# Kernel tuning notes

Hardware: AMD Instinct MI355X
Metric: run time of the kernel (lower is better)

The kernel has to match this reference:

```python
import jax, jax.numpy as jnp
import numpy as np

H = 128   # hidden_dim
M = 8     # mix_dim
N = 20000 # num_nodes
E = 320000

def gelu(x):
    return jax.nn.gelu(x, approximate=False)  # torch F.gelu default is exact erf

def setup_inputs() -> dict:
    key = jax.random.key(0)
    k1, k2, k3, k4 = jax.random.split(key, 4)
    X = jax.random.normal(k1, (N, H), dtype=jnp.float32)
    edge_index = jax.random.randint(k2, (2, E), 0, N, dtype=jnp.int64)
    # Linear weights, torch layout: y = x @ W.T
    W_A = jax.random.normal(k3, (H, H), dtype=jnp.float32) / np.sqrt(H)
    W_B = jax.random.normal(k4, (M, H), dtype=jnp.float32) / np.sqrt(H)
    return {"X": X, "edge_index": edge_index, "W_A": W_A, "W_B": W_B, "num_nodes": N}

def reference(X, edge_index, W_A, W_B, num_nodes):
    src, dst = edge_index[0], edge_index[1]
    X_src = X[src]                                   # (E, h) gather
    # compute_W_tar: W_B(gelu(W_A(X_src))), input_activation=False
    W_tar_edge = gelu(X_src @ W_A.T) @ W_B.T         # (E, m)
    # per-edge outer product, scatter_add over dst
    cross = jnp.einsum('eh,em->ehm', X_src, W_tar_edge)          # (E, h, m)
    agg = jax.ops.segment_sum(cross, dst, num_segments=num_nodes) # (N, h, m)
    agg = gelu(agg)
    # gather agg back to edges, contract over mix dim
    out_edge = jnp.einsum('ehm,em->eh', agg[dst], W_tar_edge)     # (E, h)
    # scatter_mean over dst
    ones = jnp.ones((dst.shape[0],), dtype=X.dtype)
    count = jax.ops.segment_sum(ones, dst, num_segments=num_nodes)
    out_sum = jax.ops.segment_sum(out_edge, dst, num_segments=num_nodes)
    out = out_sum / jnp.maximum(count, 1.0)[:, None]
    return out
```

## Files before the change

kernel.cpp:

```cpp
#include <hip/hip_runtime.h>
#include <hip/hip_bf16.h>


#define H 128
#define MDIM 8
#define CAP 64

typedef float v2f __attribute__((ext_vector_type(2)));

__device__ __forceinline__ float gelu_f(float x) {
    float x2 = x * x;
    float u  = x * (0.7978845608f + 0.0356774081f * x2);
    float u2 = u * u;
    float num = u * (945.0f + u2 * (105.0f + u2));
    float den = 945.0f + u2 * (420.0f + 15.0f * u2);
    float t = num * __builtin_amdgcn_rcpf(den);
    t = fminf(fmaxf(t, -1.0f), 1.0f);
    return 0.5f * (x + x * t);
}

__device__ __forceinline__ v2f gelu2(v2f x) {
    v2f x2 = x * x;
    v2f u  = x * (0.7978845608f + 0.0356774081f * x2);
    v2f u2 = u * u;
    v2f num = u * (945.0f + u2 * (105.0f + u2));
    v2f den = 945.0f + u2 * (420.0f + 15.0f * u2);
    v2f t;
    t.x = num.x * __builtin_amdgcn_rcpf(den.x);
    t.y = num.y * __builtin_amdgcn_rcpf(den.y);
    t.x = fminf(fmaxf(t.x, -1.0f), 1.0f);
    t.y = fminf(fmaxf(t.y, -1.0f), 1.0f);
    return 0.5f * (x + x * t);
}

__global__ __launch_bounds__(128) void k_prep_fill(const float* __restrict__ X,
                                                   const float* __restrict__ WA,
                                                   const float* __restrict__ WB,
                                                   const int* __restrict__ ei,
                                                   float* __restrict__ T,
                                                   int* __restrict__ cnt,
                                                   int* __restrict__ bucket,
                                                   int N, int E) {
    __shared__ float Xs[32][68];
    __shared__ float Ws[128][68];
    __shared__ float WBs[8][132];
    const int t  = threadIdx.x;
    const int n0 = blockIdx.x * 32;
    const int tn = t >> 4;
    const int tj = t & 15;

    #pragma unroll
    for (int i = 0; i < 2; ++i) {
        int idx = t + 128 * i;
        int r = idx >> 5, c4 = idx & 31;
        *(float4*)&WBs[r][c4 * 4] = *(const float4*)(WB + (size_t)r * H + c4 * 4);
    }

    float acc[4][8] = {};

    for (int kh = 0; kh < 2; ++kh) {
        __syncthreads();
        const int kb = kh * 64;
        #pragma unroll
        for (int i = 0; i < 4; ++i) {
            int idx = t + 128 * i;
            int r = idx >> 4, c4 = idx & 15;
            *(float4*)&Xs[r][c4 * 4] =
                *(const float4*)(X + (size_t)(n0 + r) * H + kb + c4 * 4);
        }
        #pragma unroll
        for (int i = 0; i < 16; ++i) {
            int idx = t + 128 * i;
            int r = idx >> 4, c4 = idx & 15;
            *(float4*)&Ws[r][c4 * 4] =
                *(const float4*)(WA + (size_t)r * H + kb + c4 * 4);
        }
        __syncthreads();

        #pragma unroll 1
        for (int k = 0; k < 64; k += 4) {
            float4 xv[4], bv[8];
            #pragma unroll
            for (int nn = 0; nn < 4; ++nn)
                xv[nn] = *(const float4*)&Xs[4 * tn + nn][k];
            #pragma unroll
            for (int jj = 0; jj < 8; ++jj)
                bv[jj] = *(const float4*)&Ws[tj + 16 * jj][k];
            #pragma unroll
            for (int nn = 0; nn < 4; ++nn)
                #pragma unroll
                for (int jj = 0; jj < 8; ++jj)
                    acc[nn][jj] += xv[nn].x * bv[jj].x + xv[nn].y * bv[jj].y +
                                   xv[nn].z * bv[jj].z + xv[nn].w * bv[jj].w;
        }
    }

    __syncthreads();
    float (*Hs)[132] = (float(*)[132])Ws;
    #pragma unroll
    for (int nn = 0; nn < 4; ++nn)
        #pragma unroll
        for (int jj = 0; jj < 8; ++jj)
            Hs[4 * tn + nn][tj + 16 * jj] = gelu_f(acc[nn][jj]);
    __syncthreads();

    #pragma unroll
    for (int i = 0; i < 2; ++i) {
        int q = t + 128 * i;
        int n = q >> 3, m = q & 7;
        float s = 0.f;
        #pragma unroll 4
        for (int kk = 0; kk < 32; ++kk) {
            float4 h = *(const float4*)&Hs[n][kk * 4];
            float4 w = *(const float4*)&WBs[m][kk * 4];
            s += h.x * w.x + h.y * w.y + h.z * w.z + h.w * w.w;
        }
        T[(size_t)(n0 + n) * MDIM + m] = s;
    }

    {
        const int stride = gridDim.x * 128;
        for (int e = blockIdx.x * 128 + t; e < E; e += stride) {
            int s  = ei[e];
            int dd = ei[E + e];
            int p  = atomicAdd(&cnt[dd], 1);
            if (p < CAP) bucket[dd * CAP + p] = s;
        }
    }
}

__device__ __forceinline__ void fma8v(v2f* acc, v2f xv, float4 ta, float4 tb) {
    acc[0] += xv * ta.x;
    acc[1] += xv * ta.y;
    acc[2] += xv * ta.z;
    acc[3] += xv * ta.w;
    acc[4] += xv * tb.x;
    acc[5] += xv * tb.y;
    acc[6] += xv * tb.z;
    acc[7] += xv * tb.w;
}

__global__ __launch_bounds__(256) void k_main(const float* __restrict__ X,
                                              const float* __restrict__ T,
                                              const int* __restrict__ cnt,
                                              const int* __restrict__ bucket,
                                              float* __restrict__ out, int N) {
    __shared__ __attribute__((aligned(16))) int srcs[4][CAP];
    __shared__ float Tl[4][CAP][MDIM];
    const int w    = threadIdx.x >> 6;
    const int lane = threadIdx.x & 63;
    const int d    = blockIdx.x * 4 + w;
    if (d >= N) return;

    const int c  = cnt[d];
    const int cc = (c < CAP) ? c : CAP;

    if (lane < cc) {
        int s = bucket[d * CAP + lane];
        srcs[w][lane] = s;
        const float4* t4 = (const float4*)(T + (size_t)s * MDIM);
        *(float4*)&Tl[w][lane][0] = t4[0];
        *(float4*)&Tl[w][lane][4] = t4[1];
    }

    float sp = 0.f;
    {
        const int m = lane & 7, g = lane >> 3;
        for (int j = g; j < cc; j += 8) sp += Tl[w][j][m];
        sp += __shfl_xor(sp, 8);
        sp += __shfl_xor(sp, 16);
        sp += __shfl_xor(sp, 32);
    }
    float S[MDIM];
    #pragma unroll
    for (int m = 0; m < MDIM; ++m) S[m] = __shfl(sp, m);

    v2f acc[MDIM] = {};
    const float* Xl = X + 2 * lane;

    int j = 0;
    for (; j + 8 <= cc; j += 8) {
        int4 sa = *(const int4*)&srcs[w][j];
        int4 sb = *(const int4*)&srcs[w][j + 4];
        v2f x0 = *(const v2f*)(Xl + (size_t)sa.x * H);
        v2f x1 = *(const v2f*)(Xl + (size_t)sa.y * H);
        v2f x2 = *(const v2f*)(Xl + (size_t)sa.z * H);
        v2f x3 = *(const v2f*)(Xl + (size_t)sa.w * H);
        v2f x4 = *(const v2f*)(Xl + (size_t)sb.x * H);
        v2f x5 = *(const v2f*)(Xl + (size_t)sb.y * H);
        v2f x6 = *(const v2f*)(Xl + (size_t)sb.z * H);
        v2f x7 = *(const v2f*)(Xl + (size_t)sb.w * H);
        #pragma unroll
        for (int q = 0; q < 8; ++q) {
            float4 ta = *(const float4*)&Tl[w][j + q][0];
            float4 tb = *(const float4*)&Tl[w][j + q][4];
            v2f xv = (q == 0) ? x0 : (q == 1) ? x1 : (q == 2) ? x2 : (q == 3) ? x3
                   : (q == 4) ? x4 : (q == 5) ? x5 : (q == 6) ? x6 : x7;
            fma8v(acc, xv, ta, tb);
        }
    }
    for (; j + 4 <= cc; j += 4) {
        int4 s4 = *(const int4*)&srcs[w][j];
        v2f x0 = *(const v2f*)(Xl + (size_t)s4.x * H);
        v2f x1 = *(const v2f*)(Xl + (size_t)s4.y * H);
        v2f x2 = *(const v2f*)(Xl + (size_t)s4.z * H);
        v2f x3 = *(const v2f*)(Xl + (size_t)s4.w * H);
        fma8v(acc, x0, *(const float4*)&Tl[w][j + 0][0], *(const float4*)&Tl[w][j + 0][4]);
        fma8v(acc, x1, *(const float4*)&Tl[w][j + 1][0], *(const float4*)&Tl[w][j + 1][4]);
        fma8v(acc, x2, *(const float4*)&Tl[w][j + 2][0], *(const float4*)&Tl[w][j + 2][4]);
        fma8v(acc, x3, *(const float4*)&Tl[w][j + 3][0], *(const float4*)&Tl[w][j + 3][4]);
    }
    for (; j < cc; ++j) {
        int s = srcs[w][j];
        v2f xv = *(const v2f*)(Xl + (size_t)s * H);
        float4 ta = *(const float4*)&Tl[w][j][0];
        float4 tb = *(const float4*)&Tl[w][j][4];
        fma8v(acc, xv, ta, tb);
    }

    v2f r = {0.f, 0.f};
    if (c > 0) {
        float inv = __builtin_amdgcn_rcpf((float)c);
        #pragma unroll
        for (int m = 0; m < MDIM; ++m) r += gelu2(acc[m]) * S[m];
        r.x *= inv;
        r.y *= inv;
    }
    *(v2f*)(out + (size_t)d * H + 2 * lane) = r;
}

extern "C" void kernel_launch(void* const* d_in, const int* in_sizes, int n_in,
                              void* d_out, int out_size, void* d_ws, size_t ws_size,
                              hipStream_t stream) {
    const float* X  = (const float*)d_in[0];
    const int*   ei = (const int*)d_in[1];
    const float* WA = (const float*)d_in[2];
    const float* WB = (const float*)d_in[3];
    float* out = (float*)d_out;

    const int N = in_sizes[0] / H;
    const int E = in_sizes[1] / 2;

    char* wp = (char*)d_ws;
    float* T    = (float*)wp;  wp += (size_t)N * MDIM * sizeof(float);
    int*   cnt  = (int*)wp;    wp += (size_t)((N + 3) & ~3) * sizeof(int);
    int*   bucket = (int*)wp;

    hipMemsetAsync(cnt, 0, (size_t)N * sizeof(int), stream);
    k_prep_fill<<<dim3(N / 32), dim3(128), 0, stream>>>(
        X, WA, WB, ei, T, cnt, bucket, N, E);
    k_main<<<dim3((N + 3) / 4), dim3(256), 0, stream>>>(X, T, cnt, bucket, out, N);
}
```

Measured before the change: 126.7 us.

## Split mix dim across half-waves with float4 gathers and packed FMA in GEMM

In k_main, each wave now splits the 8 mix channels into two halves of 4. Each of the 32 lanes per half gathers a float4 of the source row instead of a v2f, and the two halves are combined with a cross-half shuffle before a single float4 store. This uses wider gather loads, fewer accumulators per lane and fewer Tl reads, at the cost of duplicated X loads across the two halves, an extra shuffle, and removal of the 4-wide tail loop. The prep GEMM and the W_B projection are also rewritten to accumulate in v2f so the compiler can emit packed FMA, which changes the summation order.

```diff
diff --git a/kernel.cpp b/kernel.cpp
--- a/kernel.cpp
+++ b/kernel.cpp
@@ -56,7 +56,7 @@
         *(float4*)&WBs[r][c4 * 4] = *(const float4*)(WB + (size_t)r * H + c4 * 4);
     }
 
-    float acc[4][8] = {};
+    v2f accv[4][8] = {};
 
     for (int kh = 0; kh < 2; ++kh) {
         __syncthreads();
@@ -79,19 +79,26 @@
 
         #pragma unroll 1
         for (int k = 0; k < 64; k += 4) {
-            float4 xv[4], bv[8];
+            v2f xa[4][2], ba[8][2];
             #pragma unroll
-            for (int nn = 0; nn < 4; ++nn)
-                xv[nn] = *(const float4*)&Xs[4 * tn + nn][k];
+            for (int nn = 0; nn < 4; ++nn) {
+                float4 xv = *(const float4*)&Xs[4 * tn + nn][k];
+                xa[nn][0] = (v2f){xv.x, xv.y};
+                xa[nn][1] = (v2f){xv.z, xv.w};
+            }
             #pragma unroll
-            for (int jj = 0; jj < 8; ++jj)
-                bv[jj] = *(const float4*)&Ws[tj + 16 * jj][k];
+            for (int jj = 0; jj < 8; ++jj) {
+                float4 bv = *(const float4*)&Ws[tj + 16 * jj][k];
+                ba[jj][0] = (v2f){bv.x, bv.y};
+                ba[jj][1] = (v2f){bv.z, bv.w};
+            }
             #pragma unroll
             for (int nn = 0; nn < 4; ++nn)
                 #pragma unroll
-                for (int jj = 0; jj < 8; ++jj)
-                    acc[nn][jj] += xv[nn].x * bv[jj].x + xv[nn].y * bv[jj].y +
-                                   xv[nn].z * bv[jj].z + xv[nn].w * bv[jj].w;
+                for (int jj = 0; jj < 8; ++jj) {
+                    accv[nn][jj] += xa[nn][0] * ba[jj][0];
+                    accv[nn][jj] += xa[nn][1] * ba[jj][1];
+                }
         }
     }
 
@@ -101,21 +108,22 @@
     for (int nn = 0; nn < 4; ++nn)
         #pragma unroll
         for (int jj = 0; jj < 8; ++jj)
-            Hs[4 * tn + nn][tj + 16 * jj] = gelu_f(acc[nn][jj]);
+            Hs[4 * tn + nn][tj + 16 * jj] = gelu_f(accv[nn][jj].x + accv[nn][jj].y);
     __syncthreads();
 
     #pragma unroll
     for (int i = 0; i < 2; ++i) {
         int q = t + 128 * i;
         int n = q >> 3, m = q & 7;
-        float s = 0.f;
+        v2f sv = {0.f, 0.f};
         #pragma unroll 4
         for (int kk = 0; kk < 32; ++kk) {
             float4 h = *(const float4*)&Hs[n][kk * 4];
             float4 w = *(const float4*)&WBs[m][kk * 4];
-            s += h.x * w.x + h.y * w.y + h.z * w.z + h.w * w.w;
-        }
-        T[(size_t)(n0 + n) * MDIM + m] = s;
+            sv += (v2f){h.x, h.y} * (v2f){w.x, w.y};
+            sv += (v2f){h.z, h.w} * (v2f){w.z, w.w};
+        }
+        T[(size_t)(n0 + n) * MDIM + m] = sv.x + sv.y;
     }
 
     {
@@ -127,17 +135,6 @@
             if (p < CAP) bucket[dd * CAP + p] = s;
         }
     }
-}
-
-__device__ __forceinline__ void fma8v(v2f* acc, v2f xv, float4 ta, float4 tb) {
-    acc[0] += xv * ta.x;
-    acc[1] += xv * ta.y;
-    acc[2] += xv * ta.z;
-    acc[3] += xv * ta.w;
-    acc[4] += xv * tb.x;
-    acc[5] += xv * tb.y;
-    acc[6] += xv * tb.z;
-    acc[7] += xv * tb.w;
 }
 
 __global__ __launch_bounds__(256) void k_main(const float* __restrict__ X,
@@ -171,62 +168,72 @@
         sp += __shfl_xor(sp, 16);
         sp += __shfl_xor(sp, 32);
     }
-    float S[MDIM];
-    #pragma unroll
-    for (int m = 0; m < MDIM; ++m) S[m] = __shfl(sp, m);
-
-    v2f acc[MDIM] = {};
-    const float* Xl = X + 2 * lane;
+
+    const int hq = lane & 31;
+    const int mh = lane >> 5;
+    float Sv[4];
+    #pragma unroll
+    for (int mm = 0; mm < 4; ++mm) Sv[mm] = __shfl(sp, 4 * mh + mm);
+
+    v2f a0[4] = {};
+    v2f a1[4] = {};
+    const float* Xl = X + 4 * hq;
 
     int j = 0;
     for (; j + 8 <= cc; j += 8) {
         int4 sa = *(const int4*)&srcs[w][j];
         int4 sb = *(const int4*)&srcs[w][j + 4];
-        v2f x0 = *(const v2f*)(Xl + (size_t)sa.x * H);
-        v2f x1 = *(const v2f*)(Xl + (size_t)sa.y * H);
-        v2f x2 = *(const v2f*)(Xl + (size_t)sa.z * H);
-        v2f x3 = *(const v2f*)(Xl + (size_t)sa.w * H);
-        v2f x4 = *(const v2f*)(Xl + (size_t)sb.x * H);
-        v2f x5 = *(const v2f*)(Xl + (size_t)sb.y * H);
-        v2f x6 = *(const v2f*)(Xl + (size_t)sb.z * H);
-        v2f x7 = *(const v2f*)(Xl + (size_t)sb.w * H);
+        float4 x0 = *(const float4*)(Xl + (size_t)sa.x * H);
+        float4 x1 = *(const float4*)(Xl + (size_t)sa.y * H);
+        float4 x2 = *(const float4*)(Xl + (size_t)sa.z * H);
+        float4 x3 = *(const float4*)(Xl + (size_t)sa.w * H);
+        float4 x4 = *(const float4*)(Xl + (size_t)sb.x * H);
+        float4 x5 = *(const float4*)(Xl + (size_t)sb.y * H);
+        float4 x6 = *(const float4*)(Xl + (size_t)sb.z * H);
+        float4 x7 = *(const float4*)(Xl + (size_t)sb.w * H);
         #pragma unroll
         for (int q = 0; q < 8; ++q) {
-            float4 ta = *(const float4*)&Tl[w][j + q][0];
-            float4 tb = *(const float4*)&Tl[w][j + q][4];
-            v2f xv = (q == 0) ? x0 : (q == 1) ? x1 : (q == 2) ? x2 : (q == 3) ? x3
-                   : (q == 4) ? x4 : (q == 5) ? x5 : (q == 6) ? x6 : x7;
-            fma8v(acc, xv, ta, tb);
-        }
-    }
-    for (; j + 4 <= cc; j += 4) {
-        int4 s4 = *(const int4*)&srcs[w][j];
-        v2f x0 = *(const v2f*)(Xl + (size_t)s4.x * H);
-        v2f x1 = *(const v2f*)(Xl + (size_t)s4.y * H);
-        v2f x2 = *(const v2f*)(Xl + (size_t)s4.z * H);
-        v2f x3 = *(const v2f*)(Xl + (size_t)s4.w * H);
-        fma8v(acc, x0, *(const float4*)&Tl[w][j + 0][0], *(const float4*)&Tl[w][j + 0][4]);
-        fma8v(acc, x1, *(const float4*)&Tl[w][j + 1][0], *(const float4*)&Tl[w][j + 1][4]);
-        fma8v(acc, x2, *(const float4*)&Tl[w][j + 2][0], *(const float4*)&Tl[w][j + 2][4]);
-        fma8v(acc, x3, *(const float4*)&Tl[w][j + 3][0], *(const float4*)&Tl[w][j + 3][4]);
+            float4 xq = (q == 0) ? x0 : (q == 1) ? x1 : (q == 2) ? x2 : (q == 3) ? x3
+                      : (q == 4) ? x4 : (q == 5) ? x5 : (q == 6) ? x6 : x7;
+            float4 tq = *(const float4*)&Tl[w][j + q][4 * mh];
+            v2f xlo = {xq.x, xq.y}, xhi = {xq.z, xq.w};
+            a0[0] += xlo * tq.x;  a1[0] += xhi * tq.x;
+            a0[1] += xlo * tq.y;  a1[1] += xhi * tq.y;
+            a0[2] += xlo * tq.z;  a1[2] += xhi * tq.z;
+            a0[3] += xlo * tq.w;  a1[3] += xhi * tq.w;
+        }
     }
     for (; j < cc; ++j) {
         int s = srcs[w][j];
-        v2f xv = *(const v2f*)(Xl + (size_t)s * H);
-        float4 ta = *(const float4*)&Tl[w][j][0];
-        float4 tb = *(const float4*)&Tl[w][j][4];
-        fma8v(acc, xv, ta, tb);
-    }
-
-    v2f r = {0.f, 0.f};
+        float4 xq = *(const float4*)(Xl + (size_t)s * H);
+        float4 tq = *(const float4*)&Tl[w][j][4 * mh];
+        v2f xlo = {xq.x, xq.y}, xhi = {xq.z, xq.w};
+        a0[0] += xlo * tq.x;  a1[0] += xhi * tq.x;
+        a0[1] += xlo * tq.y;  a1[1] += xhi * tq.y;
+        a0[2] += xlo * tq.z;  a1[2] += xhi * tq.z;
+        a0[3] += xlo * tq.w;  a1[3] += xhi * tq.w;
+    }
+
+    float4 ro = {0.f, 0.f, 0.f, 0.f};
     if (c > 0) {
+        v2f r01 = {0.f, 0.f}, r23 = {0.f, 0.f};
+        #pragma unroll
+        for (int mm = 0; mm < 4; ++mm) {
+            r01 += gelu2(a0[mm]) * Sv[mm];
+            r23 += gelu2(a1[mm]) * Sv[mm];
+        }
+        r01.x += __shfl_xor(r01.x, 32);
+        r01.y += __shfl_xor(r01.y, 32);
+        r23.x += __shfl_xor(r23.x, 32);
+        r23.y += __shfl_xor(r23.y, 32);
         float inv = __builtin_amdgcn_rcpf((float)c);
-        #pragma unroll
-        for (int m = 0; m < MDIM; ++m) r += gelu2(acc[m]) * S[m];
-        r.x *= inv;
-        r.y *= inv;
-    }
-    *(v2f*)(out + (size_t)d * H + 2 * lane) = r;
+        ro.x = r01.x * inv;
+        ro.y = r01.y * inv;
+        ro.z = r23.x * inv;
+        ro.w = r23.y * inv;
+    }
+    if (mh == 0)
+        *(float4*)(out + (size_t)d * H + 4 * hq) = ro;
 }
 
 extern "C" void kernel_launch(void* const* d_in, const int* in_sizes, int n_in,
```

New measurement: 128.0 us. No clear change (+1.0%).
